# Performance work log

Measured on AMD Instinct MI355X. Metric: run time of the kernel, lower is better.

## Reference

```python
import jax, jax.numpy as jnp
import numpy as np

D_MODEL = 1024
D_INNER = 2048      # expand=2
D_STATE = 128
NHEADS = 32
HEADDIM = 64
DCONV = 4
CONV_DIM = D_INNER + 2 * D_STATE                 # x, B, C channels through conv
D_IN_PROJ = 2 * D_INNER + 2 * D_STATE + NHEADS   # z, xBC, dt
NBLOCKS = 4


def _mlp(x, w1, b1, w2, b2):
    # MLP(2, in, out): Linear(in,in) -> ReLU -> Linear(in,out)
    return jax.nn.relu(x @ w1 + b1) @ w2 + b2


def _mamba2_block(u, Wi, cw, cb, dtb, Alog, Dsk, nw, Wo):
    B, L, _ = u.shape
    zxbcdt = u @ Wi                                        # [B,L,D_IN_PROJ]
    z, xBC, dt = jnp.split(zxbcdt, [D_INNER, D_INNER + CONV_DIM], axis=-1)
    # causal depthwise conv1d, kernel 4
    pad = jnp.pad(xBC, ((0, 0), (DCONV - 1, 0), (0, 0)))
    conv = cb
    for k in range(DCONV):
        conv = conv + pad[:, k:k + L, :] * cw[:, k]
    xBC = jax.nn.silu(conv)
    xh, Bm, Cm = jnp.split(xBC, [D_INNER, D_INNER + D_STATE], axis=-1)
    dt = jax.nn.softplus(dt + dtb)                         # [B,L,H]
    A = -jnp.exp(Alog)                                     # [H], negative
    xh = xh.reshape(B, L, NHEADS, HEADDIM)

    def step(h, inp):
        x_t, dt_t, b_t, c_t = inp                          # [B,H,P],[B,H],[B,N],[B,N]
        dA = jnp.exp(dt_t * A)                             # [B,H]
        h = h * dA[..., None, None] + (dt_t[..., None] * x_t)[..., None] * b_t[:, None, None, :]
        y = jnp.einsum('bhpn,bn->bhp', h, c_t)
        return h, y

    h0 = jnp.zeros((B, NHEADS, HEADDIM, D_STATE), u.dtype)
    _, ys = jax.lax.scan(step, h0, (xh.transpose(1, 0, 2, 3), dt.transpose(1, 0, 2),
                                    Bm.transpose(1, 0, 2), Cm.transpose(1, 0, 2)))
    y = ys.transpose(1, 0, 2, 3) + Dsk[None, None, :, None] * xh   # D skip per head
    y = y.reshape(B, L, D_INNER)
    y = y * jax.nn.silu(z)                                 # gated RMSNorm (gate before norm)
    y = y * jax.lax.rsqrt(jnp.mean(y * y, axis=-1, keepdims=True) + 1e-5) * nw
    return y @ Wo


def setup_inputs() -> dict:
    key = jax.random.key(0)
    ks = jax.random.split(key, 16)
    B, S, STATE = 4, 512, 510
    s = 0.02
    return {
        'x': jax.random.normal(ks[0], (B, S, STATE), jnp.float32),
        'steps_left': jax.random.uniform(ks[1], (B, S, 1), jnp.float32) * 100.0,
        'current_r': jax.random.normal(ks[2], (B, S, 1), jnp.float32),
        'mlp_in_w1': jax.random.normal(ks[3], (STATE + 2, STATE + 2), jnp.float32) * s,
        'mlp_in_b1': jnp.zeros((STATE + 2,), jnp.float32),
        'mlp_in_w2': jax.random.normal(ks[4], (STATE + 2, D_MODEL), jnp.float32) * s,
        'mlp_in_b2': jnp.zeros((D_MODEL,), jnp.float32),
        'W_in': jax.random.normal(ks[5], (NBLOCKS, D_MODEL, D_IN_PROJ), jnp.float32) * s,
        'conv_w': jax.random.normal(ks[6], (NBLOCKS, CONV_DIM, DCONV), jnp.float32) * 0.2,
        'conv_b': jnp.zeros((NBLOCKS, CONV_DIM), jnp.float32),
        'dt_bias': jax.random.normal(ks[7], (NBLOCKS, NHEADS), jnp.float32) * 0.1,
        'A_log': jnp.log(jax.random.uniform(ks[8], (NBLOCKS, NHEADS), jnp.float32, 1.0, 16.0)),
        'D_skip': jnp.ones((NBLOCKS, NHEADS), jnp.float32),
        'norm_w': jnp.ones((NBLOCKS, D_INNER), jnp.float32),
        'W_out': jax.random.normal(ks[9], (NBLOCKS, D_INNER, D_MODEL), jnp.float32) * s,
        'mlp_out_w1': jax.random.normal(ks[10], (D_MODEL, D_MODEL), jnp.float32) * s,
        'mlp_out_b1': jnp.zeros((D_MODEL,), jnp.float32),
        'mlp_out_w2': jax.random.normal(ks[11], (D_MODEL, 1), jnp.float32) * s,
        'mlp_out_b2': jnp.zeros((1,), jnp.float32),
    }


def reference(x, steps_left, current_r,
              mlp_in_w1, mlp_in_b1, mlp_in_w2, mlp_in_b2,
              W_in, conv_w, conv_b, dt_bias, A_log, D_skip, norm_w, W_out,
              mlp_out_w1, mlp_out_b1, mlp_out_w2, mlp_out_b2):
    h = jnp.concatenate([x, steps_left, current_r], axis=-1)   # [B,S,state+2]
    h = _mlp(h, mlp_in_w1, mlp_in_b1, mlp_in_w2, mlp_in_b2)
    for i in range(NBLOCKS):
        h = _mamba2_block(h, W_in[i], conv_w[i], conv_b[i], dt_bias[i],
                          A_log[i], D_skip[i], norm_w[i], W_out[i])
    return _mlp(h, mlp_out_w1, mlp_out_b1, mlp_out_w2, mlp_out_b2)  # [B,S,1]
```

## Files before the change

### kernel.cpp

```cpp
#include <hip/hip_runtime.h>
#include <hip/hip_bf16.h>
#include <math.h>

#define D_MODEL   1024
#define D_INNER   2048
#define D_STATE   128
#define NHEADS    32
#define HEADDIM   64
#define DCONV     4
#define CONV_DIM  (D_INNER + 2 * D_STATE)
#define D_IN_PROJ (2 * D_INNER + 2 * D_STATE + NHEADS)
#define NBLOCKS   4
#define BATCH     4
#define SEQ       512
#define NTOK      (BATCH * SEQ)
#define STATE_IN  510
#define NPAD_IN   4480
#define NSEG      8
#define SEGLEN    64
#define NBH       (BATCH * NHEADS)
#define OFF_B     D_INNER
#define OFF_C     (D_INNER + D_STATE)
#define OFF_DT    (D_IN_PROJ - NHEADS)

typedef _Float16 half8_t __attribute__((ext_vector_type(8)));
typedef float f32x4_t  __attribute__((ext_vector_type(4)));
typedef unsigned short us;

__device__ __forceinline__ us f2h(float f) {
    _Float16 h = (_Float16)f;
    return __builtin_bit_cast(us, h);
}
__device__ __forceinline__ float h2f(us u) {
    return (float)__builtin_bit_cast(_Float16, u);
}
__device__ __forceinline__ void gl2lds16(const us* gp, us* lp) {
    __builtin_amdgcn_global_load_lds(
        (const __attribute__((address_space(1))) unsigned int*)(gp),
        (__attribute__((address_space(3))) unsigned int*)(lp), 16, 0, 0);
}

__global__ void concat_kernel(const float* __restrict__ x,
                              const float* __restrict__ steps,
                              const float* __restrict__ curr,
                              us* __restrict__ hcat)
{
    int idx = blockIdx.x * 256 + threadIdx.x;
    if (idx >= NTOK * 512) return;
    int bl = idx >> 9;
    int c  = idx & 511;
    float v;
    if (c < STATE_IN)       v = x[(size_t)bl * STATE_IN + c];
    else if (c == STATE_IN) v = steps[bl];
    else                    v = curr[bl];
    hcat[idx] = f2h(v);
}

__global__ __launch_bounds__(256)
void transpose_f16_kernel(const float* __restrict__ W, us* __restrict__ WT,
                          int K, int N)
{
    __shared__ us tile[32][36];
    int n0 = blockIdx.x * 32, k0 = blockIdx.y * 32;
    int t = threadIdx.x;
    int kl = t >> 3, nl = (t & 7) * 4;
    float4 v = make_float4(0.f, 0.f, 0.f, 0.f);
    if (n0 < N) v = *(const float4*)(W + (size_t)(k0 + kl) * N + n0 + nl);
    tile[nl + 0][kl] = f2h(v.x);
    tile[nl + 1][kl] = f2h(v.y);
    tile[nl + 2][kl] = f2h(v.z);
    tile[nl + 3][kl] = f2h(v.w);
    __syncthreads();
    int nl2 = t >> 3, kl2 = (t & 7) * 4;
    ushort4 o;
    o.x = tile[nl2][kl2 + 0];
    o.y = tile[nl2][kl2 + 1];
    o.z = tile[nl2][kl2 + 2];
    o.w = tile[nl2][kl2 + 3];
    *(ushort4*)(WT + (size_t)(n0 + nl2) * K + k0 + kl2) = o;
}

template<int BN, int TI>
__global__ __launch_bounds__(256)
void mfma_gemm_f16(const us* __restrict__ A, const us* __restrict__ BT,
                   const float* __restrict__ bias, us* __restrict__ C,
                   int N, int K, int relu)
{
    __shared__ __attribute__((aligned(16))) us Al[3][128 * 32];
    __shared__ __attribute__((aligned(16))) us Bl[3][BN * 32];
    const int tid = threadIdx.x, lane = tid & 63, wave = tid >> 6;
    const int g = lane >> 4, l16 = lane & 15;
    const int wr = (BN == 128) ? (wave >> 1) * 64 : wave * 32;
    const int wc = (BN == 128) ? (wave & 1) * 64 : 0;
    const int m0 = blockIdx.y * 128, n0 = blockIdx.x * BN;
    const int lrow = lane >> 2;
    const int lcol = ((lane & 3) ^ ((lrow >> 2) & 3)) * 8;

    f32x4_t acc[TI][4];
    const f32x4_t zero = {0.f, 0.f, 0.f, 0.f};
#pragma unroll
    for (int i = 0; i < TI; ++i)
#pragma unroll
        for (int j = 0; j < 4; ++j) acc[i][j] = zero;

    const us* abase = A  + (size_t)m0 * K;
    const us* bbase = BT + (size_t)n0 * K;

    auto stage = [&](int buf, int k0) {
#pragma unroll
        for (int s = 0; s < 2; ++s) {
            int rb = wave * 32 + s * 16;
            gl2lds16(abase + (size_t)(rb + lrow) * K + k0 + lcol, &Al[buf][rb * 32]);
        }
#pragma unroll
        for (int s = 0; s < BN / 64; ++s) {
            int rb = wave * (BN / 4) + s * 16;
            gl2lds16(bbase + (size_t)(rb + lrow) * K + k0 + lcol, &Bl[buf][rb * 32]);
        }
    };

    const int NT = K >> 5;
    stage(0, 0);
    stage(1, 32);

    int cur = 0;
    for (int t = 0; t < NT; ++t) {
        if (t == NT - 1) {
            asm volatile("s_waitcnt vmcnt(0)" ::: "memory");
        } else if constexpr (BN == 128) {
            asm volatile("s_waitcnt vmcnt(4)" ::: "memory");
        } else {
            asm volatile("s_waitcnt vmcnt(3)" ::: "memory");
        }
        __builtin_amdgcn_s_barrier();
        if (t + 2 < NT) {
            int s2 = cur + 2; if (s2 >= 3) s2 -= 3;
            stage(s2, (t + 2) << 5);
        }

        half8_t af[TI], bfr[4];
#pragma unroll
        for (int ti = 0; ti < TI; ++ti) {
            int r = wr + ti * 16 + l16;
            af[ti] = *(const half8_t*)&Al[cur][r * 32 + ((g ^ ((r >> 2) & 3)) * 8)];
        }
#pragma unroll
        for (int tj = 0; tj < 4; ++tj) {
            int r = wc + tj * 16 + l16;
            bfr[tj] = *(const half8_t*)&Bl[cur][r * 32 + ((g ^ ((r >> 2) & 3)) * 8)];
        }
#pragma unroll
        for (int ti = 0; ti < TI; ++ti)
#pragma unroll
            for (int tj = 0; tj < 4; ++tj)
                acc[ti][tj] = __builtin_amdgcn_mfma_f32_16x16x32_f16(
                    af[ti], bfr[tj], acc[ti][tj], 0, 0, 0);

        cur = (cur == 2) ? 0 : cur + 1;
    }

#pragma unroll
    for (int tj = 0; tj < 4; ++tj) {
        int col = n0 + wc + tj * 16 + l16;
        if (col >= N) continue;
        float bv = bias ? bias[col] : 0.f;
#pragma unroll
        for (int ti = 0; ti < TI; ++ti) {
            int rbase = m0 + wr + ti * 16 + g * 4;
#pragma unroll
            for (int r = 0; r < 4; ++r) {
                float v = acc[ti][tj][r] + bv;
                if (relu) v = fmaxf(v, 0.f);
                C[(size_t)(rbase + r) * N + col] = f2h(v);
            }
        }
    }
}

__global__ void conv_silu_kernel(const us* __restrict__ zxbcdt,
                                 const float* __restrict__ cw,
                                 const float* __restrict__ cb,
                                 us* __restrict__ xBCc)
{
    int idx = blockIdx.x * 256 + threadIdx.x;
    if (idx >= NTOK * CONV_DIM) return;
    int c  = idx % CONV_DIM;
    int bl = idx / CONV_DIM;
    int b  = bl >> 9;
    int l  = bl & 511;
    float acc = cb[c];
#pragma unroll
    for (int k = 0; k < DCONV; ++k) {
        int ll = l + k - (DCONV - 1);
        if (ll >= 0)
            acc = fmaf(h2f(zxbcdt[(size_t)(b * SEQ + ll) * D_IN_PROJ + D_INNER + c]),
                       cw[c * DCONV + k], acc);
    }
    xBCc[idx] = f2h(acc / (1.f + expf(-acc)));
}

__global__ __launch_bounds__(256)
void scan_seg_mfma_kernel(const us* __restrict__ zx, const us* __restrict__ xc,
                          const float* __restrict__ dt_bias,
                          const float* __restrict__ A_log,
                          const float* __restrict__ D_skip,
                          float* __restrict__ y, float* __restrict__ alpha,
                          us* __restrict__ Hseg)
{
    __shared__ __attribute__((aligned(16))) us Csh[64 * 128];
    __shared__ __attribute__((aligned(16))) us Bsh[64 * 128];
    __shared__ __attribute__((aligned(16))) us Bt[128 * 64];
    __shared__ __attribute__((aligned(16))) us Xt[64 * 64];
    __shared__ float dt_s[64], ls[64], csc[64];
    us* Ssh = Csh;
    const int bi = blockIdx.x, bh = bi >> 3, seg = bi & 7;
    const int b = bh >> 5, h = bh & 31;
    const int tid = threadIdx.x, lane = tid & 63, w = tid >> 6;
    const int g = lane >> 4, l16 = lane & 15;
    const int t0g = seg * SEGLEN;
    const size_t rowbase = (size_t)(b * SEQ + t0g);

    {
        int rr = lane >> 4, s = lane & 15;
#pragma unroll
        for (int it = 0; it < 4; ++it) {
            int rb = w * 16 + it * 4;
            int row = rb + rr;
            const us* src = xc + (rowbase + row) * CONV_DIM;
            int sw = (s ^ (row & 7)) * 8;
            gl2lds16(src + OFF_C + sw, &Csh[rb * 128]);
            gl2lds16(src + OFF_B + sw, &Bsh[rb * 128]);
        }
    }
#pragma unroll
    for (int qi = 0; qi < 4; ++qi) {
        int idx = tid + qi * 256;
        int pq = idx & 15, j = idx >> 4;
        ushort4 v = *(const ushort4*)(xc + (rowbase + j) * CONV_DIM + h * 64 + pq * 4);
#pragma unroll
        for (int e = 0; e < 4; ++e) {
            int p = pq * 4 + e;
            int pc = ((((j >> 3) ^ (p & 7)) << 3) | (j & 7));
            Xt[p * 64 + pc] = ((const us*)&v)[e];
        }
    }
#pragma unroll
    for (int qi = 0; qi < 8; ++qi) {
        int idx = tid + qi * 256;
        int nq = idx & 31, j = idx >> 5;
        ushort4 v = *(const ushort4*)(xc + (rowbase + j) * CONV_DIM + OFF_B + nq * 4);
#pragma unroll
        for (int e = 0; e < 4; ++e) {
            int n = nq * 4 + e;
            int pc = ((((j >> 3) ^ (n & 7)) << 3) | (j & 7));
            Bt[n * 64 + pc] = ((const us*)&v)[e];
        }
    }
    if (tid < 64) {
        int j = tid;
        float dtraw = h2f(zx[(rowbase + j) * D_IN_PROJ + OFF_DT + h]) + dt_bias[h];
        float dtv = (dtraw > 20.f) ? dtraw : log1pf(expf(dtraw));
        float ld = dtv * (-expf(A_log[h]));
#pragma unroll
        for (int o = 1; o < 64; o <<= 1) {
            float v = __shfl_up(ld, o);
            if (j >= o) ld += v;
        }
        float al = expf(ld);
        dt_s[j] = dtv;
        ls[j] = ld;
        alpha[(size_t)bh * SEQ + t0g + j] = al;
        float cend = __shfl(ld, 63);
        csc[j] = dtv * expf(cend - ld);
    }
    __syncthreads();

    const float Dsk = D_skip[h];
    const f32x4_t vzero = {0.f, 0.f, 0.f, 0.f};

    f32x4_t acc1[4];
#pragma unroll
    for (int jt = 0; jt < 4; ++jt) acc1[jt] = vzero;
    {
        int ia = w * 16 + l16;
#pragma unroll
        for (int ks = 0; ks < 4; ++ks) {
            half8_t a = *(const half8_t*)&Csh[ia * 128 + (((ks * 4 + g) ^ (ia & 7)) << 3)];
#pragma unroll
            for (int jt = 0; jt < 4; ++jt) {
                int jr = jt * 16 + l16;
                half8_t bfr = *(const half8_t*)&Bsh[jr * 128 + (((ks * 4 + g) ^ (jr & 7)) << 3)];
                acc1[jt] = __builtin_amdgcn_mfma_f32_16x16x32_f16(a, bfr, acc1[jt], 0, 0, 0);
            }
        }
    }
    __syncthreads();

    {
        int i0 = w * 16 + g * 4;
        float lsi[4];
#pragma unroll
        for (int r = 0; r < 4; ++r) lsi[r] = ls[i0 + r];
#pragma unroll
        for (int jt = 0; jt < 4; ++jt) {
            int j = jt * 16 + l16;
            float lj = ls[j], dj = dt_s[j];
#pragma unroll
            for (int r = 0; r < 4; ++r) {
                int i = i0 + r;
                float v = 0.f;
                if (j < i)       v = acc1[jt][r] * dj * expf(lsi[r] - lj);
                else if (j == i) v = acc1[jt][r] * dj + Dsk;
                int pc = ((((j >> 3) ^ (i & 7)) << 3) | (j & 7));
                Ssh[i * 64 + pc] = f2h(v);
            }
        }
    }
    __syncthreads();

    f32x4_t acc2[4];
#pragma unroll
    for (int nt = 0; nt < 4; ++nt) acc2[nt] = vzero;
    {
        int ia = w * 16 + l16;
#pragma unroll
        for (int ks = 0; ks < 2; ++ks) {
            half8_t a = *(const half8_t*)&Ssh[ia * 64 + (((ks * 4 + g) ^ (ia & 7)) << 3)];
#pragma unroll
            for (int nt = 0; nt < 4; ++nt) {
                int pr = nt * 16 + l16;
                half8_t bfr = *(const half8_t*)&Xt[pr * 64 + (((ks * 4 + g) ^ (pr & 7)) << 3)];
                acc2[nt] = __builtin_amdgcn_mfma_f32_16x16x32_f16(a, bfr, acc2[nt], 0, 0, 0);
            }
        }
    }
    {
        int i0 = w * 16 + g * 4;
#pragma unroll
        for (int nt = 0; nt < 4; ++nt) {
            int p = nt * 16 + l16;
#pragma unroll
            for (int r = 0; r < 4; ++r)
                y[(rowbase + i0 + r) * D_INNER + h * 64 + p] = acc2[nt][r];
        }
    }
    f32x4_t acc3[8];
#pragma unroll
    for (int nt = 0; nt < 8; ++nt) acc3[nt] = vzero;
    {
        int pa = w * 16 + l16;
#pragma unroll
        for (int ks = 0; ks < 2; ++ks) {
            half8_t araw = *(const half8_t*)&Xt[pa * 64 + (((ks * 4 + g) ^ (pa & 7)) << 3)];
            half8_t a;
#pragma unroll
            for (int e = 0; e < 8; ++e)
                a[e] = (_Float16)((float)araw[e] * csc[ks * 32 + g * 8 + e]);
#pragma unroll
            for (int nt = 0; nt < 8; ++nt) {
                int nr = nt * 16 + l16;
                half8_t bfr = *(const half8_t*)&Bt[nr * 64 + (((ks * 4 + g) ^ (nr & 7)) << 3)];
                acc3[nt] = __builtin_amdgcn_mfma_f32_16x16x32_f16(a, bfr, acc3[nt], 0, 0, 0);
            }
        }
    }
    {
        int p0 = w * 16 + g * 4;
#pragma unroll
        for (int nt = 0; nt < 8; ++nt) {
            int n = nt * 16 + l16;
#pragma unroll
            for (int r = 0; r < 4; ++r)
                Hseg[((size_t)bi * 64 + p0 + r) * 128 + n] = f2h(acc3[nt][r]);
        }
    }
}

__global__ __launch_bounds__(512)
void state_fixup_kernel(const float* __restrict__ alpha, us* __restrict__ Hseg)
{
    const int bh = blockIdx.x;
    const int t = threadIdx.x, p = t >> 3, ng = t & 7;
    float carry[16];
#pragma unroll
    for (int j = 0; j < 16; ++j) carry[j] = 0.f;
    for (int seg = 0; seg < NSEG; ++seg) {
        us* hs = Hseg + (((size_t)bh * NSEG + seg) * 64 + p) * 128;
        float ae = alpha[(size_t)bh * SEQ + seg * SEGLEN + SEGLEN - 1];
        float tmp[16];
#pragma unroll
        for (int q = 0; q < 4; ++q) {
            ushort4 u = *(const ushort4*)(hs + ng * 4 + q * 32);
            tmp[q*4+0] = h2f(u.x); tmp[q*4+1] = h2f(u.y);
            tmp[q*4+2] = h2f(u.z); tmp[q*4+3] = h2f(u.w);
        }
#pragma unroll
        for (int q = 0; q < 4; ++q) {
            ushort4 o;
            o.x = f2h(carry[q*4+0]); o.y = f2h(carry[q*4+1]);
            o.z = f2h(carry[q*4+2]); o.w = f2h(carry[q*4+3]);
            *(ushort4*)(hs + ng * 4 + q * 32) = o;
        }
#pragma unroll
        for (int j = 0; j < 16; ++j) carry[j] = fmaf(carry[j], ae, tmp[j]);
    }
}

__global__ __launch_bounds__(256)
void correct_mfma_kernel(const us* __restrict__ xc, const float* __restrict__ alpha,
                         const us* __restrict__ Hseg, float* __restrict__ y)
{
    __shared__ __attribute__((aligned(16))) us Csh[64 * 128];
    __shared__ __attribute__((aligned(16))) us Hsh[64 * 128];
    __shared__ float als_s[64];
    const int bi = blockIdx.x;
    const int bh = bi / 7, seg = 1 + (bi % 7);
    const int b = bh >> 5, h = bh & 31;
    const int tid = threadIdx.x, lane = tid & 63, w = tid >> 6;
    const int g = lane >> 4, l16 = lane & 15;
    const int t0g = seg * SEGLEN;
    const size_t rowbase = (size_t)(b * SEQ + t0g);
    const size_t hbase = (size_t)(bh * NSEG + seg) * 64;

    {
        int rr = lane >> 4, s = lane & 15;
#pragma unroll
        for (int it = 0; it < 4; ++it) {
            int rb = w * 16 + it * 4;
            int row = rb + rr;
            int sw = (s ^ (row & 7)) * 8;
            gl2lds16(xc + (rowbase + row) * CONV_DIM + OFF_C + sw, &Csh[rb * 128]);
            gl2lds16(Hseg + (hbase + row) * 128 + sw, &Hsh[rb * 128]);
        }
    }
    if (tid < 64) als_s[tid] = alpha[(size_t)bh * SEQ + t0g + tid];
    __syncthreads();

    const f32x4_t vzero = {0.f, 0.f, 0.f, 0.f};
    f32x4_t acc[4];
#pragma unroll
    for (int nt = 0; nt < 4; ++nt) acc[nt] = vzero;
    int ia = w * 16 + l16;
#pragma unroll
    for (int ks = 0; ks < 4; ++ks) {
        half8_t a = *(const half8_t*)&Csh[ia * 128 + (((ks * 4 + g) ^ (ia & 7)) << 3)];
#pragma unroll
        for (int nt = 0; nt < 4; ++nt) {
            int pr = nt * 16 + l16;
            half8_t bfr = *(const half8_t*)&Hsh[pr * 128 + (((ks * 4 + g) ^ (pr & 7)) << 3)];
            acc[nt] = __builtin_amdgcn_mfma_f32_16x16x32_f16(a, bfr, acc[nt], 0, 0, 0);
        }
    }
    int i0 = w * 16 + g * 4;
#pragma unroll
    for (int nt = 0; nt < 4; ++nt) {
        int p = nt * 16 + l16;
#pragma unroll
        for (int r = 0; r < 4; ++r) {
            size_t idx = (rowbase + i0 + r) * D_INNER + h * 64 + p;
            y[idx] += als_s[i0 + r] * acc[nt][r];
        }
    }
}

__global__ __launch_bounds__(256)
void gated_rmsnorm_kernel(const float* __restrict__ y,
                          const us* __restrict__ zxbcdt,
                          const float* __restrict__ norm_w,
                          us* __restrict__ yn)
{
    int bl = blockIdx.x;
    int t  = threadIdx.x;
    const float* yr = y + (size_t)bl * D_INNER;
    const us* zr = zxbcdt + (size_t)bl * D_IN_PROJ;
    us* outr = yn + (size_t)bl * D_INNER;

    float gv[8];
    float ss = 0.f;
#pragma unroll
    for (int q = 0; q < 8; ++q) {
        int j = t + q * 256;
        float z = h2f(zr[j]);
        float g = yr[j] * (z / (1.f + expf(-z)));
        gv[q] = g;
        ss += g * g;
    }
    __shared__ float red[256];
    red[t] = ss;
    __syncthreads();
    for (int w = 128; w > 0; w >>= 1) {
        if (t < w) red[t] += red[t + w];
        __syncthreads();
    }
    float rs = rsqrtf(red[0] / (float)D_INNER + 1e-5f);
#pragma unroll
    for (int q = 0; q < 8; ++q) {
        int j = t + q * 256;
        outr[j] = f2h(gv[q] * rs * norm_w[j]);
    }
}

__global__ __launch_bounds__(256)
void final_dot_kernel(const us* __restrict__ t1,
                      const float* __restrict__ w2,
                      const float* __restrict__ b2,
                      float* __restrict__ out)
{
    int bl = blockIdx.x;
    int t  = threadIdx.x;
    float s = 0.f;
    for (int j = t; j < D_MODEL; j += 256)
        s = fmaf(h2f(t1[(size_t)bl * D_MODEL + j]), w2[j], s);
    __shared__ float red[256];
    red[t] = s;
    __syncthreads();
    for (int w = 128; w > 0; w >>= 1) {
        if (t < w) red[t] += red[t + w];
        __syncthreads();
    }
    if (t == 0) out[bl] = red[0] + b2[0];
}

extern "C" void kernel_launch(void* const* d_in, const int* in_sizes, int n_in,
                              void* d_out, int out_size, void* d_ws, size_t ws_size,
                              hipStream_t stream)
{
    const float* x        = (const float*)d_in[0];
    const float* steps    = (const float*)d_in[1];
    const float* curr     = (const float*)d_in[2];
    const float* mi_w1    = (const float*)d_in[3];
    const float* mi_b1    = (const float*)d_in[4];
    const float* mi_w2    = (const float*)d_in[5];
    const float* mi_b2    = (const float*)d_in[6];
    const float* W_in     = (const float*)d_in[7];
    const float* conv_w   = (const float*)d_in[8];
    const float* conv_b   = (const float*)d_in[9];
    const float* dt_bias  = (const float*)d_in[10];
    const float* A_log    = (const float*)d_in[11];
    const float* D_skip   = (const float*)d_in[12];
    const float* norm_w   = (const float*)d_in[13];
    const float* W_out    = (const float*)d_in[14];
    const float* mo_w1    = (const float*)d_in[15];
    const float* mo_b1    = (const float*)d_in[16];
    const float* mo_w2    = (const float*)d_in[17];
    const float* mo_b2    = (const float*)d_in[18];
    float* out = (float*)d_out;

    us* wt_mi1 = (us*)d_ws;
    us* wt_mi2 = wt_mi1 + (size_t)512 * 512;
    us* wt_in  = wt_mi2 + (size_t)1024 * 512;
    us* wt_out = wt_in  + (size_t)4 * NPAD_IN * 1024;
    us* wt_mo1 = wt_out + (size_t)4 * 1024 * 2048;
    us* Hseg   = wt_mo1 + (size_t)1024 * 1024;
    us* hcat   = Hseg   + (size_t)NBH * NSEG * 64 * 128;
    us* h      = hcat   + (size_t)NTOK * 512;
    us* zxb    = h      + (size_t)NTOK * D_MODEL;
    us* xc     = zxb    + (size_t)NTOK * D_IN_PROJ;
    us* yn     = xc     + (size_t)NTOK * CONV_DIM;
    us* t0     = zxb;
    us* t1     = xc;
    float* fbase = (float*)((((uintptr_t)(yn + (size_t)NTOK * D_INNER)) + 255)
                            & ~(uintptr_t)255);
    float* y     = fbase;
    float* alpha = y + (size_t)NTOK * D_INNER;

    transpose_f16_kernel<<<dim3(512/32, 512/32), 256, 0, stream>>>(mi_w1, wt_mi1, 512, 512);
    transpose_f16_kernel<<<dim3(1024/32, 512/32), 256, 0, stream>>>(mi_w2, wt_mi2, 512, 1024);
    for (int i = 0; i < NBLOCKS; ++i) {
        transpose_f16_kernel<<<dim3(NPAD_IN/32, 1024/32), 256, 0, stream>>>(
            W_in + (size_t)i * D_MODEL * D_IN_PROJ, wt_in + (size_t)i * NPAD_IN * 1024,
            D_MODEL, D_IN_PROJ);
        transpose_f16_kernel<<<dim3(1024/32, 2048/32), 256, 0, stream>>>(
            W_out + (size_t)i * D_INNER * D_MODEL, wt_out + (size_t)i * 1024 * 2048,
            D_INNER, D_MODEL);
    }
    transpose_f16_kernel<<<dim3(1024/32, 1024/32), 256, 0, stream>>>(mo_w1, wt_mo1, 1024, 1024);

    concat_kernel<<<(NTOK * 512 + 255) / 256, 256, 0, stream>>>(x, steps, curr, hcat);

    mfma_gemm_f16<64, 2><<<dim3(512/64, NTOK/128), 256, 0, stream>>>(
        hcat, wt_mi1, mi_b1, t0, 512, 512, 1);
    mfma_gemm_f16<64, 2><<<dim3(1024/64, NTOK/128), 256, 0, stream>>>(
        t0, wt_mi2, mi_b2, h, 1024, 512, 0);

    for (int i = 0; i < NBLOCKS; ++i) {
        mfma_gemm_f16<128, 4><<<dim3(NPAD_IN/128, NTOK/128), 256, 0, stream>>>(
            h, wt_in + (size_t)i * NPAD_IN * 1024, nullptr, zxb, D_IN_PROJ, D_MODEL, 0);
        conv_silu_kernel<<<(NTOK * CONV_DIM + 255) / 256, 256, 0, stream>>>(
            zxb, conv_w + (size_t)i * CONV_DIM * DCONV, conv_b + (size_t)i * CONV_DIM, xc);
        scan_seg_mfma_kernel<<<NBH * NSEG, 256, 0, stream>>>(
            zxb, xc, dt_bias + i * NHEADS, A_log + i * NHEADS, D_skip + i * NHEADS,
            y, alpha, Hseg);
        state_fixup_kernel<<<NBH, 512, 0, stream>>>(alpha, Hseg);
        correct_mfma_kernel<<<NBH * (NSEG - 1), 256, 0, stream>>>(xc, alpha, Hseg, y);
        gated_rmsnorm_kernel<<<NTOK, 256, 0, stream>>>(
            y, zxb, norm_w + (size_t)i * D_INNER, yn);
        mfma_gemm_f16<64, 2><<<dim3(1024/64, NTOK/128), 256, 0, stream>>>(
            yn, wt_out + (size_t)i * 1024 * 2048, nullptr, h, 1024, 2048, 0);
    }

    mfma_gemm_f16<64, 2><<<dim3(1024/64, NTOK/128), 256, 0, stream>>>(
        h, wt_mo1, mo_b1, t1, 1024, 1024, 1);
    final_dot_kernel<<<NTOK, 256, 0, stream>>>(t1, mo_w2, mo_b2, out);
}
```

Baseline: 787.8 us.

## Merge weight transposes into one launch, unroll GEMM ring, vectorize conv, fast exp

All per-matrix weight transpose launches are replaced by a single kernel that uses a flat block index to pick the source matrix and tile, cutting launch count. The GEMM main loop is unrolled by three so the triple-buffer indices are compile-time constants. The causal conv+SiLU kernel now handles four channels per thread with vector loads of the inputs, weights and bias. expf is swapped for __expf in the conv, scan and norm kernels, which trades a little accuracy for cheaper exponentials.

```diff
diff --git a/kernel.cpp b/kernel.cpp
--- a/kernel.cpp
+++ b/kernel.cpp
@@ -56,12 +56,37 @@
     hcat[idx] = f2h(v);
 }
 
+#define NT_TRANS 27904
 __global__ __launch_bounds__(256)
-void transpose_f16_kernel(const float* __restrict__ W, us* __restrict__ WT,
-                          int K, int N)
-{
+void transpose_all_kernel(const float* __restrict__ mi_w1, const float* __restrict__ mi_w2,
+                          const float* __restrict__ W_in, const float* __restrict__ W_out,
+                          const float* __restrict__ mo_w1,
+                          us* __restrict__ wt_mi1, us* __restrict__ wt_mi2,
+                          us* __restrict__ wt_in, us* __restrict__ wt_out,
+                          us* __restrict__ wt_mo1)
+{
+    int bid = blockIdx.x;
+    const float* W; us* WT; int K, N, ntx, r;
+    if (bid < 256)        { W = mi_w1; WT = wt_mi1; K = 512;  N = 512;  ntx = 16;  r = bid; }
+    else if (bid < 768)   { W = mi_w2; WT = wt_mi2; K = 512;  N = 1024; ntx = 32;  r = bid - 256; }
+    else if (bid < 18688) {
+        int rel = bid - 768, i = rel / 4480;
+        r = rel - i * 4480;
+        W  = W_in  + (size_t)i * D_MODEL * D_IN_PROJ;
+        WT = wt_in + (size_t)i * NPAD_IN * 1024;
+        K = 1024; N = D_IN_PROJ; ntx = 140;
+    }
+    else if (bid < 26880) {
+        int rel = bid - 18688, i = rel / 2048;
+        r = rel - i * 2048;
+        W  = W_out  + (size_t)i * D_INNER * D_MODEL;
+        WT = wt_out + (size_t)i * 1024 * 2048;
+        K = 2048; N = 1024; ntx = 32;
+    }
+    else { W = mo_w1; WT = wt_mo1; K = 1024; N = 1024; ntx = 32; r = bid - 26880; }
+    int n0 = (r % ntx) * 32, k0 = (r / ntx) * 32;
+
     __shared__ us tile[32][36];
-    int n0 = blockIdx.x * 32, k0 = blockIdx.y * 32;
     int t = threadIdx.x;
     int kl = t >> 3, nl = (t & 7) * 4;
     float4 v = make_float4(0.f, 0.f, 0.f, 0.f);
@@ -80,6 +105,35 @@
     *(ushort4*)(WT + (size_t)(n0 + nl2) * K + k0 + kl2) = o;
 }
 
+#define PHASE(TT, CUR, STG)                                                     \
+    {                                                                           \
+        if ((TT) == NT - 1)                                                     \
+            asm volatile("s_waitcnt vmcnt(0)" ::: "memory");                    \
+        else if constexpr (BN == 128)                                           \
+            asm volatile("s_waitcnt vmcnt(4)" ::: "memory");                    \
+        else                                                                    \
+            asm volatile("s_waitcnt vmcnt(3)" ::: "memory");                    \
+        __builtin_amdgcn_s_barrier();                                           \
+        if ((TT) + 2 < NT) stage(STG, ((TT) + 2) << 5);                         \
+        half8_t af[TI], bfr[4];                                                 \
+        _Pragma("unroll")                                                       \
+        for (int ti = 0; ti < TI; ++ti) {                                       \
+            int rr = wr + ti * 16 + l16;                                        \
+            af[ti] = *(const half8_t*)&Al[CUR][rr * 32 + ((g ^ ((rr >> 2) & 3)) * 8)]; \
+        }                                                                       \
+        _Pragma("unroll")                                                       \
+        for (int tj = 0; tj < 4; ++tj) {                                        \
+            int rr = wc + tj * 16 + l16;                                        \
+            bfr[tj] = *(const half8_t*)&Bl[CUR][rr * 32 + ((g ^ ((rr >> 2) & 3)) * 8)]; \
+        }                                                                       \
+        _Pragma("unroll")                                                       \
+        for (int ti = 0; ti < TI; ++ti)                                         \
+            _Pragma("unroll")                                                   \
+            for (int tj = 0; tj < 4; ++tj)                                      \
+                acc[ti][tj] = __builtin_amdgcn_mfma_f32_16x16x32_f16(           \
+                    af[ti], bfr[tj], acc[ti][tj], 0, 0, 0);                     \
+    }
+
 template<int BN, int TI>
 __global__ __launch_bounds__(256)
 void mfma_gemm_f16(const us* __restrict__ A, const us* __restrict__ BT,
@@ -123,40 +177,10 @@
     stage(0, 0);
     stage(1, 32);
 
-    int cur = 0;
-    for (int t = 0; t < NT; ++t) {
-        if (t == NT - 1) {
-            asm volatile("s_waitcnt vmcnt(0)" ::: "memory");
-        } else if constexpr (BN == 128) {
-            asm volatile("s_waitcnt vmcnt(4)" ::: "memory");
-        } else {
-            asm volatile("s_waitcnt vmcnt(3)" ::: "memory");
-        }
-        __builtin_amdgcn_s_barrier();
-        if (t + 2 < NT) {
-            int s2 = cur + 2; if (s2 >= 3) s2 -= 3;
-            stage(s2, (t + 2) << 5);
-        }
-
-        half8_t af[TI], bfr[4];
-#pragma unroll
-        for (int ti = 0; ti < TI; ++ti) {
-            int r = wr + ti * 16 + l16;
-            af[ti] = *(const half8_t*)&Al[cur][r * 32 + ((g ^ ((r >> 2) & 3)) * 8)];
-        }
-#pragma unroll
-        for (int tj = 0; tj < 4; ++tj) {
-            int r = wc + tj * 16 + l16;
-            bfr[tj] = *(const half8_t*)&Bl[cur][r * 32 + ((g ^ ((r >> 2) & 3)) * 8)];
-        }
-#pragma unroll
-        for (int ti = 0; ti < TI; ++ti)
-#pragma unroll
-            for (int tj = 0; tj < 4; ++tj)
-                acc[ti][tj] = __builtin_amdgcn_mfma_f32_16x16x32_f16(
-                    af[ti], bfr[tj], acc[ti][tj], 0, 0, 0);
-
-        cur = (cur == 2) ? 0 : cur + 1;
+    for (int t = 0; t < NT; t += 3) {
+        PHASE(t, 0, 2)
+        if (t + 1 < NT) PHASE(t + 1, 1, 0)
+        if (t + 2 < NT) PHASE(t + 2, 2, 1)
     }
 
 #pragma unroll
@@ -177,26 +201,43 @@
     }
 }
 
-__global__ void conv_silu_kernel(const us* __restrict__ zxbcdt,
-                                 const float* __restrict__ cw,
-                                 const float* __restrict__ cb,
-                                 us* __restrict__ xBCc)
+__global__ __launch_bounds__(256)
+void conv_silu_kernel(const us* __restrict__ zxbcdt,
+                      const float* __restrict__ cw,
+                      const float* __restrict__ cb,
+                      us* __restrict__ xBCc)
 {
     int idx = blockIdx.x * 256 + threadIdx.x;
-    if (idx >= NTOK * CONV_DIM) return;
-    int c  = idx % CONV_DIM;
-    int bl = idx / CONV_DIM;
+    if (idx >= NTOK * (CONV_DIM / 4)) return;
+    int cq = idx % (CONV_DIM / 4);
+    int bl = idx / (CONV_DIM / 4);
     int b  = bl >> 9;
     int l  = bl & 511;
-    float acc = cb[c];
+    int c  = cq * 4;
+    float4 w0 = *(const float4*)&cw[(c + 0) * DCONV];
+    float4 w1 = *(const float4*)&cw[(c + 1) * DCONV];
+    float4 w2 = *(const float4*)&cw[(c + 2) * DCONV];
+    float4 w3 = *(const float4*)&cw[(c + 3) * DCONV];
+    float4 bb = *(const float4*)&cb[c];
+    float a0 = bb.x, a1 = bb.y, a2 = bb.z, a3 = bb.w;
+    const us* base = zxbcdt + (size_t)(b * SEQ) * D_IN_PROJ + D_INNER + c;
 #pragma unroll
     for (int k = 0; k < DCONV; ++k) {
         int ll = l + k - (DCONV - 1);
-        if (ll >= 0)
-            acc = fmaf(h2f(zxbcdt[(size_t)(b * SEQ + ll) * D_IN_PROJ + D_INNER + c]),
-                       cw[c * DCONV + k], acc);
-    }
-    xBCc[idx] = f2h(acc / (1.f + expf(-acc)));
+        if (ll >= 0) {
+            ushort4 u = *(const ushort4*)(base + (size_t)ll * D_IN_PROJ);
+            a0 = fmaf(h2f(u.x), ((const float*)&w0)[k], a0);
+            a1 = fmaf(h2f(u.y), ((const float*)&w1)[k], a1);
+            a2 = fmaf(h2f(u.z), ((const float*)&w2)[k], a2);
+            a3 = fmaf(h2f(u.w), ((const float*)&w3)[k], a3);
+        }
+    }
+    ushort4 o;
+    o.x = f2h(a0 / (1.f + __expf(-a0)));
+    o.y = f2h(a1 / (1.f + __expf(-a1)));
+    o.z = f2h(a2 / (1.f + __expf(-a2)));
+    o.w = f2h(a3 / (1.f + __expf(-a3)));
+    *(ushort4*)(xBCc + (size_t)bl * CONV_DIM + c) = o;
 }
 
 __global__ __launch_bounds__(256)
@@ -309,7 +350,7 @@
             for (int r = 0; r < 4; ++r) {
                 int i = i0 + r;
                 float v = 0.f;
-                if (j < i)       v = acc1[jt][r] * dj * expf(lsi[r] - lj);
+                if (j < i)       v = acc1[jt][r] * dj * __expf(lsi[r] - lj);
                 else if (j == i) v = acc1[jt][r] * dj + Dsk;
                 int pc = ((((j >> 3) ^ (i & 7)) << 3) | (j & 7));
                 Ssh[i * 64 + pc] = f2h(v);
@@ -481,7 +522,7 @@
     for (int q = 0; q < 8; ++q) {
         int j = t + q * 256;
         float z = h2f(zr[j]);
-        float g = yr[j] * (z / (1.f + expf(-z)));
+        float g = yr[j] * (z / (1.f + __expf(-z)));
         gv[q] = g;
         ss += g * g;
     }
@@ -564,17 +605,9 @@
     float* y     = fbase;
     float* alpha = y + (size_t)NTOK * D_INNER;
 
-    transpose_f16_kernel<<<dim3(512/32, 512/32), 256, 0, stream>>>(mi_w1, wt_mi1, 512, 512);
-    transpose_f16_kernel<<<dim3(1024/32, 512/32), 256, 0, stream>>>(mi_w2, wt_mi2, 512, 1024);
-    for (int i = 0; i < NBLOCKS; ++i) {
-        transpose_f16_kernel<<<dim3(NPAD_IN/32, 1024/32), 256, 0, stream>>>(
-            W_in + (size_t)i * D_MODEL * D_IN_PROJ, wt_in + (size_t)i * NPAD_IN * 1024,
-            D_MODEL, D_IN_PROJ);
-        transpose_f16_kernel<<<dim3(1024/32, 2048/32), 256, 0, stream>>>(
-            W_out + (size_t)i * D_INNER * D_MODEL, wt_out + (size_t)i * 1024 * 2048,
-            D_INNER, D_MODEL);
-    }
-    transpose_f16_kernel<<<dim3(1024/32, 1024/32), 256, 0, stream>>>(mo_w1, wt_mo1, 1024, 1024);
+    transpose_all_kernel<<<NT_TRANS, 256, 0, stream>>>(
+        mi_w1, mi_w2, W_in, W_out, mo_w1,
+        wt_mi1, wt_mi2, wt_in, wt_out, wt_mo1);
 
     concat_kernel<<<(NTOK * 512 + 255) / 256, 256, 0, stream>>>(x, steps, curr, hcat);
 
@@ -586,7 +619,7 @@
     for (int i = 0; i < NBLOCKS; ++i) {
         mfma_gemm_f16<128, 4><<<dim3(NPAD_IN/128, NTOK/128), 256, 0, stream>>>(
             h, wt_in + (size_t)i * NPAD_IN * 1024, nullptr, zxb, D_IN_PROJ, D_MODEL, 0);
-        conv_silu_kernel<<<(NTOK * CONV_DIM + 255) / 256, 256, 0, stream>>>(
+        conv_silu_kernel<<<(NTOK * (CONV_DIM/4) + 255) / 256, 256, 0, stream>>>(
             zxb, conv_w + (size_t)i * CONV_DIM * DCONV, conv_b + (size_t)i * CONV_DIM, xc);
         scan_seg_mfma_kernel<<<NBH * NSEG, 256, 0, stream>>>(
             zxb, xc, dt_bias + i * NHEADS, A_log + i * NHEADS, D_skip + i * NHEADS,
```

Measured after the change: 747.9 us. 1.05x faster.
